# Kernel tuning notes

Measured on AMD Instinct MI355X. Metric: run time of the kernel, lower is better.

## Reference

```python
import jax, jax.numpy as jnp
import numpy as np

B, N, IN, H, DK, DV, OUT = 8, 1024, 512, 8, 64, 64, 512
SCALE = 1.0 / (DK ** 0.5)


def setup_inputs() -> dict:
    key = jax.random.key(0)
    ks = jax.random.split(key, 10)
    s = lambda fan_in: 1.0 / np.sqrt(fan_in)
    return {
        "x": jax.random.normal(ks[0], (B, N, IN), dtype=jnp.float32),
        "Wv": jax.random.uniform(ks[1], (IN, H * DV), jnp.float32, -s(IN), s(IN)),
        "bv": jax.random.uniform(ks[2], (H * DV,), jnp.float32, -s(IN), s(IN)),
        "Wk": jax.random.uniform(ks[3], (IN, H * DK), jnp.float32, -s(IN), s(IN)),
        "bk": jax.random.uniform(ks[4], (H * DK,), jnp.float32, -s(IN), s(IN)),
        "Wq": jax.random.uniform(ks[5], (IN, H * DK), jnp.float32, -s(IN), s(IN)),
        "bq": jax.random.uniform(ks[6], (H * DK,), jnp.float32, -s(IN), s(IN)),
        "Wo": jax.random.uniform(ks[7], (H * DV, OUT), jnp.float32, -s(H * DV), s(H * DV)),
        "bo": jax.random.uniform(ks[8], (OUT,), jnp.float32, -s(H * DV), s(H * DV)),
        "mask": jax.random.randint(ks[9], (B, N, N), 0, 2, dtype=jnp.int32),
    }


def reference(x, Wv, bv, Wk, bk, Wq, bq, Wo, bo, mask):
    # projections -> (B, N, H, d), vkq activation = relu
    v = jax.nn.relu((x @ Wv + bv).reshape(B, N, H, DV))
    q = jax.nn.relu((x @ Wq + bq).reshape(B, N, H, DK))
    k = jax.nn.relu((x @ Wk + bk).reshape(B, N, H, DK))
    # (B, H, N, d)
    q, k, v = (t.transpose(0, 2, 1, 3) for t in (q, k, v))
    # raw attention weights (returned pre-mask, pre-softmax): (B, H, N, N)
    att_weights = jnp.einsum("bhqd,bhkd->bhqk", q, k) * SCALE
    att = jnp.where(mask[:, None, :, :] == 0, -1e9, att_weights)
    att = jax.nn.softmax(att, axis=-1)
    out = jnp.einsum("bhqk,bhkd->bhqd", att, v) + v  # residual add of v
    out = out.transpose(0, 2, 1, 3).reshape(B, N, H * DV)
    out = jax.nn.relu(out @ Wo + bo)  # final activation = relu
    return out, att_weights
```

## Files before the change

kernel.cpp:

```cpp
#include <hip/hip_runtime.h>
#include <hip/hip_bf16.h>

typedef __attribute__((ext_vector_type(8))) short short8;
typedef __attribute__((ext_vector_type(4))) float f32x4;

#define DEV static __device__ __forceinline__

DEV unsigned short f2bf(float f) {
  union { float f; unsigned u; } v; v.f = f;
  unsigned r = v.u + 0x7FFFu + ((v.u >> 16) & 1u);
  return (unsigned short)(r >> 16);
}
DEV float bf2f(unsigned short b) {
  union { unsigned u; float f; } v; v.u = ((unsigned)b) << 16;
  return v.f;
}

DEV unsigned cvtpk_bf16(float lo, float hi) {
  unsigned r;
  asm("v_cvt_pk_bf16_f32 %0, %1, %2" : "=v"(r) : "v"(lo), "v"(hi));
  return r;
}

DEV void gld_lds16(const void* g, void* l) {
  __builtin_amdgcn_global_load_lds(
      (const __attribute__((address_space(1))) unsigned int*)g,
      (__attribute__((address_space(3))) unsigned int*)l, 16, 0, 0);
}

DEV short8 lds_read8(const unsigned short* base, int byteoff) {
  return *reinterpret_cast<const short8*>(reinterpret_cast<const char*>(base) + byteoff);
}

__global__ __launch_bounds__(256) void prep_kernel(
    const float* __restrict__ x, unsigned short* __restrict__ xb,
    const float* __restrict__ W0, const float* __restrict__ W1,
    const float* __restrict__ W2, const float* __restrict__ W3,
    unsigned short* __restrict__ T0, unsigned short* __restrict__ T1,
    unsigned short* __restrict__ T2, unsigned short* __restrict__ T3,
    const int* __restrict__ mask, unsigned char* __restrict__ mb) {
  __shared__ unsigned short tile[32][33];
  const int bid = blockIdx.x, tid = threadIdx.x;
  if (bid < 4096) {
    int i = bid * 256 + tid;
    float4 v = reinterpret_cast<const float4*>(x)[i];
    ushort4 o;
    o.x = f2bf(v.x); o.y = f2bf(v.y); o.z = f2bf(v.z); o.w = f2bf(v.w);
    reinterpret_cast<ushort4*>(xb)[i] = o;
  } else if (bid < 5120) {
    int r = bid - 4096;
    int z = r >> 8;
    r &= 255;
    const float* W = z == 0 ? W0 : z == 1 ? W1 : z == 2 ? W2 : W3;
    unsigned short* T = z == 0 ? T0 : z == 1 ? T1 : z == 2 ? T2 : T3;
    int tx = tid & 31, ty = tid >> 5;
    int n0 = (r & 15) * 32, k0 = (r >> 4) * 32;
#pragma unroll
    for (int i = 0; i < 32; i += 8)
      tile[ty + i][tx] = f2bf(W[(size_t)(k0 + ty + i) * 512 + n0 + tx]);
    __syncthreads();
#pragma unroll
    for (int i = 0; i < 32; i += 8)
      T[(size_t)(n0 + ty + i) * 512 + k0 + tx] = tile[tx][ty + i];
  } else {
    int i = (bid - 5120) * 256 + tid;
    int4 m4 = reinterpret_cast<const int4*>(mask)[i];
    unsigned v = (m4.x ? 1u : 0u) | ((m4.y ? 1u : 0u) << 8) |
                 ((m4.z ? 1u : 0u) << 16) | ((m4.w ? 1u : 0u) << 24);
    reinterpret_cast<unsigned*>(mb)[i] = v;
  }
}

__global__ __launch_bounds__(256) void mask_prep_kernel(const int* __restrict__ mask,
                                                        unsigned char* __restrict__ mb) {
  int i = blockIdx.x * 256 + threadIdx.x;
  int4 m4 = reinterpret_cast<const int4*>(mask)[i];
  unsigned v = (m4.x ? 1u : 0u) | ((m4.y ? 1u : 0u) << 8) |
               ((m4.z ? 1u : 0u) << 16) | ((m4.w ? 1u : 0u) << 24);
  reinterpret_cast<unsigned*>(mb)[i] = v;
}

__global__ __launch_bounds__(256) void gemm_proj_kernel(
    const unsigned short* __restrict__ xb,
    const unsigned short* __restrict__ WqT, const unsigned short* __restrict__ WkT,
    const unsigned short* __restrict__ WvT,
    const float* __restrict__ bq, const float* __restrict__ bk, const float* __restrict__ bv,
    unsigned short* __restrict__ qn, unsigned short* __restrict__ kn,
    unsigned short* __restrict__ vn, unsigned short* __restrict__ vT) {
  const int z = blockIdx.z;
  const unsigned short* Wt = z == 0 ? WqT : z == 1 ? WkT : WvT;
  const float* bias = z == 0 ? bq : z == 1 ? bk : bv;
  unsigned short* outp = z == 0 ? qn : z == 1 ? kn : vn;

  __shared__ unsigned short smem[17408];
  unsigned short* As = smem;
  unsigned short* Bs = smem + 8192;

  const int tid = threadIdx.x;
  const int lane = tid & 63;
  const int w = tid >> 6;
  const int wm = w >> 1, wn = w & 1;
  const int lr = lane & 15;
  const int g = lane >> 4;

  const int m0 = blockIdx.x * 128;
  const int n0 = blockIdx.y * 128;

  f32x4 acc[4][4];
#pragma unroll
  for (int i = 0; i < 4; ++i)
#pragma unroll
    for (int j = 0; j < 4; ++j) acc[i][j] = (f32x4){0.f, 0.f, 0.f, 0.f};

#define STAGE_AB(buf, k0)                                                         \
  {                                                                               \
    _Pragma("unroll") for (int p = 0; p < 2; ++p) {                               \
      int slot = tid + 256 * p;                                                   \
      int r = slot >> 2;                                                          \
      int kg = (slot & 3) ^ ((r >> 1) & 3);                                       \
      unsigned short* ldsA = As + (buf)*4096 + (size_t)(w + 4 * p) * 512;         \
      unsigned short* ldsB = Bs + (buf)*4096 + (size_t)(w + 4 * p) * 512;         \
      gld_lds16(xb + (size_t)(m0 + r) * 512 + (k0) + kg * 8, ldsA);               \
      gld_lds16(Wt + (size_t)(n0 + r) * 512 + (k0) + kg * 8, ldsB);               \
    }                                                                             \
  }

  STAGE_AB(0, 0)
  asm volatile("s_waitcnt vmcnt(0)" ::: "memory");
  __builtin_amdgcn_sched_barrier(0);
  __builtin_amdgcn_s_barrier();

  int cur = 0;
  for (int kt = 0; kt < 16; ++kt) {
    if (kt < 15) STAGE_AB(cur ^ 1, (kt + 1) * 32)
    __builtin_amdgcn_sched_barrier(0);

    const unsigned short* Ac = As + cur * 4096;
    const unsigned short* Bc = Bs + cur * 4096;
    short8 af[4], bfr[4];
#pragma unroll
    for (int mi = 0; mi < 4; ++mi) {
      int r = wm * 64 + mi * 16 + lr;
      af[mi] = lds_read8(Ac, (r * 64 + g * 16) ^ (((r >> 1) & 3) << 4));
    }
#pragma unroll
    for (int ni = 0; ni < 4; ++ni) {
      int r = wn * 64 + ni * 16 + lr;
      bfr[ni] = lds_read8(Bc, (r * 64 + g * 16) ^ (((r >> 1) & 3) << 4));
    }
    __builtin_amdgcn_s_setprio(1);
#pragma unroll
    for (int mi = 0; mi < 4; ++mi)
#pragma unroll
      for (int ni = 0; ni < 4; ++ni)
        acc[mi][ni] = __builtin_amdgcn_mfma_f32_16x16x32_bf16(af[mi], bfr[ni], acc[mi][ni], 0, 0, 0);
    __builtin_amdgcn_s_setprio(0);

    asm volatile("s_waitcnt vmcnt(0)" ::: "memory");
    __builtin_amdgcn_sched_barrier(0);
    __builtin_amdgcn_s_barrier();
    __builtin_amdgcn_sched_barrier(0);
    cur ^= 1;
  }

  float biasv[4];
#pragma unroll
  for (int ni = 0; ni < 4; ++ni) biasv[ni] = bias[n0 + wn * 64 + ni * 16 + lr];

#pragma unroll
  for (int mi = 0; mi < 4; ++mi) {
    int rowb = m0 + wm * 64 + mi * 16 + g * 4;
#pragma unroll
    for (int ni = 0; ni < 4; ++ni) {
      int c = n0 + wn * 64 + ni * 16 + lr;
      int h = c >> 6, d = c & 63;
#pragma unroll
      for (int rr = 0; rr < 4; ++rr) {
        float vf = acc[mi][ni][rr] + biasv[ni];
        vf = vf > 0.f ? vf : 0.f;
        unsigned short bvv = f2bf(vf);
        int row = rowb + rr;
        int b = row >> 10, tok = row & 1023;
        outp[((size_t)(b * 8 + h) * 1024 + tok) * 64 + d] = bvv;
        if (z == 2) {
          int cl = wn * 64 + ni * 16 + lr;
          int rl = wm * 64 + mi * 16 + g * 4 + rr;
          smem[cl * 136 + rl] = bvv;
        }
      }
    }
  }
  if (z == 2) {
    __syncthreads();
    int cl = tid >> 1, half = tid & 1;
    int gc = n0 + cl, h = gc >> 6, d = gc & 63;
    int b = m0 >> 10;
    int tokbase = (m0 & 1023) + half * 64;
    size_t base = (size_t)(b * 8 + h) * 65536 + (size_t)d * 1024 + tokbase;
    const unsigned short* src = smem + cl * 136 + half * 64;
#pragma unroll
    for (int j = 0; j < 8; ++j) {
      short8 v8 = *reinterpret_cast<const short8*>(src + j * 8);
      *reinterpret_cast<short8*>(vT + base + j * 8) = v8;
    }
  }
#undef STAGE_AB
}

__global__ __launch_bounds__(512) void attn_kernel(
    const unsigned short* __restrict__ qg, const unsigned short* __restrict__ kgp,
    const unsigned short* __restrict__ vg, const unsigned short* __restrict__ vTg,
    const unsigned char* __restrict__ mb, float* __restrict__ attw,
    unsigned short* __restrict__ Og) {
  __shared__ unsigned short Ks[2][4096];
  __shared__ unsigned short Vs[2][4096];
  __shared__ unsigned short Ps[8192];

  const int tid = threadIdx.x, lane = tid & 63, w = tid >> 6;
  const int lr = lane & 15, g = lane >> 4;

  const int bid = blockIdx.x;
  const int b = bid & 7;
  const int idx = bid >> 3;
  const int h = idx >> 3;
  const int qc = idx & 7;
  const int bh = b * 8 + h;

  const int qw = qc * 128 + w * 16;
  const size_t qbase = (size_t)bh * 65536;

  const unsigned short* kbase = kgp + qbase;
  const unsigned short* vbase = vTg + qbase;

  const int srow = w * 8 + (lane >> 3);
  const int ssw = ((lane & 7) ^ (srow & 7)) * 8;

  short8 aq[2];
#pragma unroll
  for (int dc = 0; dc < 2; ++dc)
    aq[dc] = *reinterpret_cast<const short8*>(
        qg + qbase + (size_t)(qw + lr) * 64 + dc * 32 + g * 8);

  f32x4 o[4];
#pragma unroll
  for (int di = 0; di < 4; ++di) o[di] = (f32x4){0.f, 0.f, 0.f, 0.f};
  float lsum = 0.f;

  unsigned short* Pw = Ps + w * 1024;
  const unsigned char* mp = mb + ((size_t)(b * 1024 + qw + lr)) * 1024 + g * 4;
  float* awp = attw + ((size_t)bh * 1024 + qw + lr) * 1024 + g * 4;

  gld_lds16(kbase + (size_t)srow * 64 + ssw, reinterpret_cast<char*>(Ks[0]) + w * 1024);
  gld_lds16(vbase + (size_t)srow * 1024 + ssw, reinterpret_cast<char*>(Vs[0]) + w * 1024);
  asm volatile("s_waitcnt vmcnt(0)" ::: "memory");
  __builtin_amdgcn_sched_barrier(0);
  __builtin_amdgcn_s_barrier();

  int cur = 0;
  for (int t = 0; t < 16; ++t) {
    const int kv0 = t * 64;

    unsigned mk[4];
#pragma unroll
    for (int ni = 0; ni < 4; ++ni)
      mk[ni] = *reinterpret_cast<const unsigned*>(mp + kv0 + ni * 16);
    __builtin_amdgcn_sched_barrier(0);

    if (t < 15) {
      const int kn0 = kv0 + 64;
      gld_lds16(kbase + (size_t)(kn0 + srow) * 64 + ssw,
                reinterpret_cast<char*>(Ks[cur ^ 1]) + w * 1024);
      gld_lds16(vbase + (size_t)srow * 1024 + kn0 + ssw,
                reinterpret_cast<char*>(Vs[cur ^ 1]) + w * 1024);
    }
    __builtin_amdgcn_sched_barrier(0);

    const unsigned short* Kc = Ks[cur];
    const unsigned short* Vc = Vs[cur];

    f32x4 s[4];
    __builtin_amdgcn_s_setprio(1);
#pragma unroll
    for (int ni = 0; ni < 4; ++ni) {
      int row = ni * 16 + lr;
      s[ni] = (f32x4){0.f, 0.f, 0.f, 0.f};
#pragma unroll
      for (int dc = 0; dc < 2; ++dc) {
        short8 ak = lds_read8(Kc, (row * 128 + dc * 64 + g * 16) ^ ((row & 7) << 4));
        s[ni] = __builtin_amdgcn_mfma_f32_16x16x32_bf16(ak, aq[dc], s[ni], 0, 0, 0);
      }
    }
    __builtin_amdgcn_s_setprio(0);

#pragma unroll
    for (int ni = 0; ni < 4; ++ni) {
      f32x4 sv = s[ni] * 0.125f;
      *reinterpret_cast<f32x4*>(awp + kv0 + ni * 16) = sv;
      unsigned m = mk[ni];
      float p0 = (m & 0x000000FFu) ? __expf(sv[0] - 16.f) : 0.f;
      float p1 = (m & 0x0000FF00u) ? __expf(sv[1] - 16.f) : 0.f;
      float p2 = (m & 0x00FF0000u) ? __expf(sv[2] - 16.f) : 0.f;
      float p3 = (m & 0xFF000000u) ? __expf(sv[3] - 16.f) : 0.f;
      lsum += (p0 + p1) + (p2 + p3);
      uint2 pk = make_uint2(cvtpk_bf16(p0, p1), cvtpk_bf16(p2, p3));
      int pbyte = (lr * 128 + ni * 32 + g * 8) ^ ((lr & 7) << 4);
      *reinterpret_cast<uint2*>(reinterpret_cast<char*>(Pw) + pbyte) = pk;
    }

    __builtin_amdgcn_s_setprio(1);
#pragma unroll
    for (int kc = 0; kc < 2; ++kc) {
      short8 ap = lds_read8(Pw, (lr * 128 + kc * 64 + g * 16) ^ ((lr & 7) << 4));
#pragma unroll
      for (int di = 0; di < 4; ++di) {
        int rd = di * 16 + lr;
        short8 bv8 = lds_read8(Vc, (rd * 128 + kc * 64 + g * 16) ^ ((rd & 7) << 4));
        o[di] = __builtin_amdgcn_mfma_f32_16x16x32_bf16(ap, bv8, o[di], 0, 0, 0);
      }
    }
    __builtin_amdgcn_s_setprio(0);

    asm volatile("s_waitcnt vmcnt(4)" ::: "memory");
    __builtin_amdgcn_sched_barrier(0);
    __builtin_amdgcn_s_barrier();
    __builtin_amdgcn_sched_barrier(0);
    cur ^= 1;
  }

  float l = lsum;
  l += __shfl_xor(l, 16);
  l += __shfl_xor(l, 32);

#pragma unroll
  for (int rr = 0; rr < 4; ++rr) {
    int gq2 = qw + g * 4 + rr;
    float lq = __shfl(l, g * 4 + rr);
    float inv = 1.f / lq;
#pragma unroll
    for (int di = 0; di < 4; ++di) {
      int gd = di * 16 + lr;
      float ov = o[di][rr] * inv + bf2f(vg[qbase + (size_t)gq2 * 64 + gd]);
      Og[((size_t)(b * 1024 + gq2)) * 512 + h * 64 + gd] = f2bf(ov);
    }
  }
}

__global__ __launch_bounds__(256) void gemm_out_kernel(
    const unsigned short* __restrict__ Ab, const unsigned short* __restrict__ WoT,
    const float* __restrict__ bo, float* __restrict__ outp) {
  __shared__ unsigned short smem[16384];
  unsigned short* As = smem;
  unsigned short* Bs = smem + 8192;

  const int tid = threadIdx.x;
  const int lane = tid & 63;
  const int w = tid >> 6;
  const int wm = w >> 1, wn = w & 1;
  const int lr = lane & 15;
  const int g = lane >> 4;
  const int m0 = blockIdx.x * 128;
  const int n0 = blockIdx.y * 128;

  f32x4 acc[4][4];
#pragma unroll
  for (int i = 0; i < 4; ++i)
#pragma unroll
    for (int j = 0; j < 4; ++j) acc[i][j] = (f32x4){0.f, 0.f, 0.f, 0.f};

#define STAGE_AB(buf, k0)                                                         \
  {                                                                               \
    _Pragma("unroll") for (int p = 0; p < 2; ++p) {                               \
      int slot = tid + 256 * p;                                                   \
      int r = slot >> 2;                                                          \
      int kg = (slot & 3) ^ ((r >> 1) & 3);                                       \
      unsigned short* ldsA = As + (buf)*4096 + (size_t)(w + 4 * p) * 512;         \
      unsigned short* ldsB = Bs + (buf)*4096 + (size_t)(w + 4 * p) * 512;         \
      gld_lds16(Ab + (size_t)(m0 + r) * 512 + (k0) + kg * 8, ldsA);               \
      gld_lds16(WoT + (size_t)(n0 + r) * 512 + (k0) + kg * 8, ldsB);              \
    }                                                                             \
  }

  STAGE_AB(0, 0)
  asm volatile("s_waitcnt vmcnt(0)" ::: "memory");
  __builtin_amdgcn_sched_barrier(0);
  __builtin_amdgcn_s_barrier();

  int cur = 0;
  for (int kt = 0; kt < 16; ++kt) {
    if (kt < 15) STAGE_AB(cur ^ 1, (kt + 1) * 32)
    __builtin_amdgcn_sched_barrier(0);

    const unsigned short* Ac = As + cur * 4096;
    const unsigned short* Bc = Bs + cur * 4096;
    short8 af[4], bfr[4];
#pragma unroll
    for (int mi = 0; mi < 4; ++mi) {
      int r = wm * 64 + mi * 16 + lr;
      af[mi] = lds_read8(Ac, (r * 64 + g * 16) ^ (((r >> 1) & 3) << 4));
    }
#pragma unroll
    for (int ni = 0; ni < 4; ++ni) {
      int r = wn * 64 + ni * 16 + lr;
      bfr[ni] = lds_read8(Bc, (r * 64 + g * 16) ^ (((r >> 1) & 3) << 4));
    }
    __builtin_amdgcn_s_setprio(1);
#pragma unroll
    for (int mi = 0; mi < 4; ++mi)
#pragma unroll
      for (int ni = 0; ni < 4; ++ni)
        acc[mi][ni] = __builtin_amdgcn_mfma_f32_16x16x32_bf16(af[mi], bfr[ni], acc[mi][ni], 0, 0, 0);
    __builtin_amdgcn_s_setprio(0);

    asm volatile("s_waitcnt vmcnt(0)" ::: "memory");
    __builtin_amdgcn_sched_barrier(0);
    __builtin_amdgcn_s_barrier();
    __builtin_amdgcn_sched_barrier(0);
    cur ^= 1;
  }
#undef STAGE_AB

  float biasv[4];
#pragma unroll
  for (int ni = 0; ni < 4; ++ni) biasv[ni] = bo[n0 + wn * 64 + ni * 16 + lr];
#pragma unroll
  for (int mi = 0; mi < 4; ++mi) {
    int rowb = m0 + wm * 64 + mi * 16 + g * 4;
#pragma unroll
    for (int ni = 0; ni < 4; ++ni) {
      int c = n0 + wn * 64 + ni * 16 + lr;
#pragma unroll
      for (int rr = 0; rr < 4; ++rr) {
        float vf = acc[mi][ni][rr] + biasv[ni];
        outp[(size_t)(rowb + rr) * 512 + c] = vf > 0.f ? vf : 0.f;
      }
    }
  }
}

extern "C" void kernel_launch(void* const* d_in, const int* in_sizes, int n_in,
                              void* d_out, int out_size, void* d_ws, size_t ws_size,
                              hipStream_t stream) {
  const float* x = (const float*)d_in[0];
  const float* Wv = (const float*)d_in[1];
  const float* bv = (const float*)d_in[2];
  const float* Wk = (const float*)d_in[3];
  const float* bk = (const float*)d_in[4];
  const float* Wq = (const float*)d_in[5];
  const float* bq = (const float*)d_in[6];
  const float* Wo = (const float*)d_in[7];
  const float* bo = (const float*)d_in[8];
  const int* mask = (const int*)d_in[9];

  char* ws = (char*)d_ws;
  unsigned short* xb  = (unsigned short*)(ws);
  unsigned short* WqT = (unsigned short*)(ws + 8388608);
  unsigned short* WkT = (unsigned short*)(ws + 8912896);
  unsigned short* WvT = (unsigned short*)(ws + 9437184);
  unsigned short* WoT = (unsigned short*)(ws + 9961472);
  unsigned short* qn  = (unsigned short*)(ws + 10485760);
  unsigned short* kn  = (unsigned short*)(ws + 18874368);
  unsigned short* vn  = (unsigned short*)(ws + 27262976);
  unsigned short* vT  = (unsigned short*)(ws + 35651584);
  unsigned short* Og  = (unsigned short*)(ws + 44040192);

  const size_t MBB_HI = 52428800;
  const bool big = ws_size >= MBB_HI + 8388608;
  unsigned char* mbb = big ? (unsigned char*)(ws + MBB_HI) : (unsigned char*)ws;

  float* outp = (float*)d_out;
  float* attw = (float*)d_out + 4194304;

  prep_kernel<<<big ? 13312 : 5120, 256, 0, stream>>>(
      x, xb, Wq, Wk, Wv, Wo, WqT, WkT, WvT, WoT, mask, mbb);

  dim3 gp(64, 4, 3);
  gemm_proj_kernel<<<gp, 256, 0, stream>>>(xb, WqT, WkT, WvT, bq, bk, bv, qn, kn, vn, vT);

  if (!big) mask_prep_kernel<<<8192, 256, 0, stream>>>(mask, mbb);

  attn_kernel<<<512, 512, 0, stream>>>(qn, kn, vn, vT, mbb, attw, Og);

  dim3 go(64, 4);
  gemm_out_kernel<<<go, 256, 0, stream>>>(Og, WoT, bo, outp);
}
```

Measured before the change: 132.4 us.

## Triple-buffer K/V tiles and prefetch mask one iteration ahead in attention

Measured after the change: 169.9 us. +28.3%, slower.

```diff
diff --git a/kernel.cpp b/kernel.cpp
--- a/kernel.cpp
+++ b/kernel.cpp
@@ -212,8 +212,8 @@
     const unsigned short* __restrict__ vg, const unsigned short* __restrict__ vTg,
     const unsigned char* __restrict__ mb, float* __restrict__ attw,
     unsigned short* __restrict__ Og) {
-  __shared__ unsigned short Ks[2][4096];
-  __shared__ unsigned short Vs[2][4096];
+  __shared__ unsigned short Ks[3][4096];
+  __shared__ unsigned short Vs[3][4096];
   __shared__ unsigned short Ps[8192];
 
   const int tid = threadIdx.x, lane = tid & 63, w = tid >> 6;
@@ -250,28 +250,41 @@
   const unsigned char* mp = mb + ((size_t)(b * 1024 + qw + lr)) * 1024 + g * 4;
   float* awp = attw + ((size_t)bh * 1024 + qw + lr) * 1024 + g * 4;
 
-  gld_lds16(kbase + (size_t)srow * 64 + ssw, reinterpret_cast<char*>(Ks[0]) + w * 1024);
-  gld_lds16(vbase + (size_t)srow * 1024 + ssw, reinterpret_cast<char*>(Vs[0]) + w * 1024);
-  asm volatile("s_waitcnt vmcnt(0)" ::: "memory");
+#define STAGE_T(kv0, buf)                                                      \
+  gld_lds16(kbase + (size_t)((kv0) + srow) * 64 + ssw,                         \
+            reinterpret_cast<char*>(Ks[buf]) + w * 1024);                      \
+  gld_lds16(vbase + (size_t)srow * 1024 + (kv0) + ssw,                         \
+            reinterpret_cast<char*>(Vs[buf]) + w * 1024);
+
+  unsigned mk[4];
+#pragma unroll
+  for (int ni = 0; ni < 4; ++ni)
+    mk[ni] = *reinterpret_cast<const unsigned*>(mp + ni * 16);
+  __builtin_amdgcn_sched_barrier(0);
+  STAGE_T(0, 0)
+  __builtin_amdgcn_sched_barrier(0);
+  STAGE_T(64, 1)
+  __builtin_amdgcn_sched_barrier(0);
+  asm volatile("s_waitcnt vmcnt(2)" ::: "memory");
   __builtin_amdgcn_sched_barrier(0);
   __builtin_amdgcn_s_barrier();
-
-  int cur = 0;
+  __builtin_amdgcn_sched_barrier(0);
+
+#pragma unroll
   for (int t = 0; t < 16; ++t) {
     const int kv0 = t * 64;
-
-    unsigned mk[4];
-#pragma unroll
-    for (int ni = 0; ni < 4; ++ni)
-      mk[ni] = *reinterpret_cast<const unsigned*>(mp + kv0 + ni * 16);
-    __builtin_amdgcn_sched_barrier(0);
-
+    const int cur = t % 3;
+
+    unsigned mkn[4];
     if (t < 15) {
-      const int kn0 = kv0 + 64;
-      gld_lds16(kbase + (size_t)(kn0 + srow) * 64 + ssw,
-                reinterpret_cast<char*>(Ks[cur ^ 1]) + w * 1024);
-      gld_lds16(vbase + (size_t)srow * 1024 + kn0 + ssw,
-                reinterpret_cast<char*>(Vs[cur ^ 1]) + w * 1024);
+#pragma unroll
+      for (int ni = 0; ni < 4; ++ni)
+        mkn[ni] = *reinterpret_cast<const unsigned*>(mp + kv0 + 64 + ni * 16);
+    }
+    __builtin_amdgcn_sched_barrier(0);
+
+    if (t < 14) {
+      STAGE_T(kv0 + 128, (t + 2) % 3)
     }
     __builtin_amdgcn_sched_barrier(0);
 
@@ -319,13 +332,26 @@
       }
     }
     __builtin_amdgcn_s_setprio(0);
-
-    asm volatile("s_waitcnt vmcnt(4)" ::: "memory");
-    __builtin_amdgcn_sched_barrier(0);
-    __builtin_amdgcn_s_barrier();
-    __builtin_amdgcn_sched_barrier(0);
-    cur ^= 1;
-  }
+    __builtin_amdgcn_sched_barrier(0);
+
+    if (t == 0) {
+      asm volatile("s_waitcnt vmcnt(10)" ::: "memory");
+    } else if (t < 14) {
+      asm volatile("s_waitcnt vmcnt(14)" ::: "memory");
+    } else if (t == 14) {
+      asm volatile("s_waitcnt vmcnt(12)" ::: "memory");
+    }
+    if (t < 15) {
+      __builtin_amdgcn_sched_barrier(0);
+      __builtin_amdgcn_s_barrier();
+      __builtin_amdgcn_sched_barrier(0);
+    }
+    if (t < 15) {
+#pragma unroll
+      for (int ni = 0; ni < 4; ++ni) mk[ni] = mkn[ni];
+    }
+  }
+#undef STAGE_T
 
   float l = lsum;
   l += __shfl_xor(l, 16);
```
